# Kernel optimization log

Measured on AMD Instinct MI355X. Metric: run time of the kernel, lower is better.

Reference implementation:

```python
import jax, jax.numpy as jnp
import numpy as np

EPS = 1e-5

def batchnorm2d(x, w, b):
    # training-mode BN: per-channel stats over (B, H, W), biased variance
    mean = jnp.mean(x, axis=(0, 2, 3), keepdims=True)
    var = jnp.var(x, axis=(0, 2, 3), keepdims=True)
    xn = (x - mean) * jax.lax.rsqrt(var + EPS)
    return xn * w[None, :, None, None] + b[None, :, None, None]

def setup_inputs() -> dict:
    key = jax.random.key(0)
    ks = jax.random.split(key, 12)
    B, C, H, W = 4, 64, 64, 64
    Cq = C // 8
    s = 1.0 / np.sqrt(C)
    return {
        "x": jax.random.normal(ks[0], (B, C, H, W), jnp.float32),
        "Wq": jax.random.normal(ks[1], (Cq, C), jnp.float32) * s,
        "bq": jnp.zeros((Cq,), jnp.float32),
        "Wk": jax.random.normal(ks[2], (Cq, C), jnp.float32) * s,
        "bk": jnp.zeros((Cq,), jnp.float32),
        "Wv": jax.random.normal(ks[3], (C, C), jnp.float32) * s,
        "bv": jnp.zeros((C,), jnp.float32),
        "gamma_p": jax.random.normal(ks[4], (), jnp.float32) * 0.1,
        "bnp_w": jnp.ones((C,), jnp.float32),
        "bnp_b": jnp.zeros((C,), jnp.float32),
        "gamma_c": jax.random.normal(ks[5], (), jnp.float32) * 0.1,
        "bnc_w": jnp.ones((C,), jnp.float32),
        "bnc_b": jnp.zeros((C,), jnp.float32),
    }

def reference(x, Wq, bq, Wk, bk, Wv, bv, gamma_p, bnp_w, bnp_b, gamma_c, bnc_w, bnc_b):
    B, C, H, W = x.shape
    N = H * W
    xf = x.reshape(B, C, N)

    # ---- PAM (position attention) ----
    q = jnp.einsum('dc,bcn->bnd', Wq, xf) + bq  # [B, N, Cq]
    k = jnp.einsum('dc,bcn->bdn', Wk, xf) + bk[None, :, None]  # [B, Cq, N]
    v = jnp.einsum('dc,bcn->bdn', Wv, xf) + bv[None, :, None]  # [B, C, N]
    energy = jnp.einsum('bnd,bdm->bnm', q, k)  # [B, N, N]
    attn = jax.nn.softmax(energy, axis=-1)
    # out[b,c,m] = sum_n v[b,c,n] * attn[m,n]  (bmm(v, attn^T))
    out = jnp.einsum('bcn,bmn->bcm', v, attn).reshape(B, C, H, W)
    out = gamma_p * out
    out = batchnorm2d(out, bnp_w, bnp_b)
    y = out + x  # PAM residual

    # ---- CAM (channel attention) ----
    yf = y.reshape(B, C, N)
    energy_c = jnp.einsum('bcn,bdn->bcd', yf, yf)  # [B, C, C]
    energy_new = jnp.max(energy_c, axis=-1, keepdims=True) - energy_c
    attn_c = jax.nn.softmax(energy_new, axis=-1)
    out_c = jnp.einsum('bcd,bdn->bcn', attn_c, yf).reshape(B, C, H, W)
    out_c = gamma_c * out_c
    out_c = batchnorm2d(out_c, bnc_w, bnc_b)
    return out_c + y  # CAM residual
```

## Files before the change

kernel.cpp:

```cpp
#include <hip/hip_runtime.h>

#define NN 4096
#define EPS 1e-5f

typedef unsigned long long u64;
union f2u { float f[2]; u64 u; };
typedef float f32x2 __attribute__((ext_vector_type(2)));
typedef float f32x4v __attribute__((ext_vector_type(4)));

#define PK_LO(acc, a, b) \
  asm("v_pk_fma_f32 %0, %1, %2, %0 op_sel:[0,0,0] op_sel_hi:[1,0,1]" \
      : "+v"(acc) : "v"(a), "v"(b))
#define PK_HI(acc, a, b) \
  asm("v_pk_fma_f32 %0, %1, %2, %0 op_sel:[0,1,0] op_sel_hi:[1,1,1]" \
      : "+v"(acc) : "v"(a), "v"(b))

#define Q_OFF   0u
#define K_OFF   131072u
#define V_OFF   262144u
#define O_OFF   1310720u
#define Y_OFF   2359296u
#define OC_OFF  3407872u
#define AT_OFF  4456448u
#define S2_OFF  4472832u
#define PS_OFF  4472960u
#define CNT_OFF 4473088u
#define OP_OFF  4473344u
#define LP_OFF  8667648u

__global__ __launch_bounds__(256) void proj_kernel(
    const float* __restrict__ x, const float* __restrict__ Wq, const float* __restrict__ bq,
    const float* __restrict__ Wk, const float* __restrict__ bk,
    const float* __restrict__ Wv, const float* __restrict__ bv,
    float* __restrict__ q, float* __restrict__ k, float* __restrict__ v) {
  __shared__ float sWq[8*64], sWk[8*64], sWv[64*64], sbq[8], sbk[8], sbv[64];
  __shared__ float xt[64*68];
  int t = threadIdx.x;
  int b = blockIdx.x >> 6;
  int sp = blockIdx.x & 63;
  int n0 = sp << 6;
  for (int i = t; i < 512; i += 256) { sWq[i] = Wq[i]; sWk[i] = Wk[i]; }
  for (int i = t; i < 4096; i += 256) sWv[i] = Wv[i];
  if (t < 64) sbv[t] = bv[t];
  if (t < 8) { sbq[t] = bq[t]; sbk[t] = bk[t]; }
  for (int i = t; i < 1024; i += 256) {
    int c = i >> 4, nf = (i & 15) << 2;
    *(float4*)&xt[c*68 + nf] =
        *(const float4*)&x[(size_t)(((b<<6)|c)<<12) + n0 + nf];
  }
  __syncthreads();
  int nl = t & 63;
  int n = n0 | nl;
  int cg_ = t >> 6;
  float xv[64];
  #pragma unroll
  for (int c = 0; c < 64; ++c) xv[c] = xt[c*68 + nl];
  for (int c = cg_*16; c < cg_*16+16; ++c) {
    float acc = sbv[c];
    #pragma unroll
    for (int c2 = 0; c2 < 64; ++c2) acc += sWv[c*64 + c2] * xv[c2];
    v[(((b<<6)|c)<<12) | n] = acc;
  }
  if (cg_ == 0) {
    #pragma unroll
    for (int d = 0; d < 8; ++d) {
      float acc = sbq[d];
      #pragma unroll
      for (int c = 0; c < 64; ++c) acc += sWq[d*64+c] * xv[c];
      q[(((b<<12)|n)<<3) | d] = acc;
    }
  } else if (cg_ == 1) {
    #pragma unroll
    for (int d = 0; d < 8; ++d) {
      float acc = sbk[d];
      #pragma unroll
      for (int c = 0; c < 64; ++c) acc += sWk[d*64+c] * xv[c];
      k[(((b<<3)|d)<<12) | n] = acc;
    }
  }
}

__global__ __launch_bounds__(256, 4) void attn_kernel(
    const float* __restrict__ q, const float* __restrict__ k,
    const float* __restrict__ v, float* __restrict__ op,
    float* __restrict__ lp, float* __restrict__ o,
    float* __restrict__ psums, int* __restrict__ cnt) {
  __shared__ float kst[64*12];
  __shared__ float vst[64*68];
  __shared__ float pst[64*68];
  __shared__ int who;

  const int bi   = blockIdx.x;
  const int g    = bi & 3;
  const int rest = bi >> 2;
  const int mt   = rest & 63;
  const int b    = rest >> 6;
  const int m0   = mt << 6;
  const int t    = threadIdx.x;

  const int rq = t & 15;
  const int sg = t >> 4;

  f32x2 qq[2][8];
  {
    f32x4v rowv[4][2];
    #pragma unroll
    for (int r = 0; r < 4; ++r) {
      const f32x4v* qp = (const f32x4v*)&q[(size_t)(((b<<12) | (m0 + (rq<<2) + r)) << 3)];
      rowv[r][0] = qp[0]; rowv[r][1] = qp[1];
    }
    #pragma unroll
    for (int p = 0; p < 2; ++p)
      #pragma unroll
      for (int j = 0; j < 8; ++j) {
        f32x2 w;
        w[0] = rowv[2*p][j>>2][j&3];
        w[1] = rowv[2*p+1][j>>2][j&3];
        qq[p][j] = w;
      }
  }

  float lsum[4] = {0.f, 0.f, 0.f, 0.f};
  f32x2 A2[4][2];
  #pragma unroll
  for (int c = 0; c < 4; ++c) { A2[c][0] = (f32x2){0.f,0.f}; A2[c][1] = (f32x2){0.f,0.f}; }

  const int span = NN >> 2;
  const int nbeg = g * span;

  for (int n0 = nbeg; n0 < nbeg + span; n0 += 64) {
    __syncthreads();
    #pragma unroll
    for (int i = t; i < 512; i += 256) {
      int ni = i & 63, d = i >> 6;
      kst[ni*12 + d] = k[(((b<<3)|d)<<12) + n0 + ni];
    }
    #pragma unroll
    for (int i = t; i < 4096; i += 256) {
      int ni = i & 63, c = i >> 6;
      vst[ni*68 + c] = v[(((b<<6)|c)<<12) + n0 + ni];
    }
    __syncthreads();
    #pragma unroll
    for (int j4 = 0; j4 < 4; ++j4) {
      const int ni = (sg << 2) | j4;
      const f32x4v ka = *(const f32x4v*)&kst[ni*12];
      const f32x4v kb = *(const f32x4v*)&kst[ni*12 + 4];
      const f32x2 k01 = __builtin_shufflevector(ka, ka, 0, 1);
      const f32x2 k23 = __builtin_shufflevector(ka, ka, 2, 3);
      const f32x2 k45 = __builtin_shufflevector(kb, kb, 0, 1);
      const f32x2 k67 = __builtin_shufflevector(kb, kb, 2, 3);
      f32x2 s01 = (f32x2){0.f,0.f}, s23 = (f32x2){0.f,0.f};
      PK_LO(s01, qq[0][0], k01); PK_HI(s01, qq[0][1], k01);
      PK_LO(s01, qq[0][2], k23); PK_HI(s01, qq[0][3], k23);
      PK_LO(s01, qq[0][4], k45); PK_HI(s01, qq[0][5], k45);
      PK_LO(s01, qq[0][6], k67); PK_HI(s01, qq[0][7], k67);
      PK_LO(s23, qq[1][0], k01); PK_HI(s23, qq[1][1], k01);
      PK_LO(s23, qq[1][2], k23); PK_HI(s23, qq[1][3], k23);
      PK_LO(s23, qq[1][4], k45); PK_HI(s23, qq[1][5], k45);
      PK_LO(s23, qq[1][6], k67); PK_HI(s23, qq[1][7], k67);
      const float e0 = __expf(s01[0]), e1 = __expf(s01[1]);
      const float e2 = __expf(s23[0]), e3 = __expf(s23[1]);
      lsum[0] += e0; lsum[1] += e1; lsum[2] += e2; lsum[3] += e3;
      *(float4*)&pst[ni*68 + (rq<<2)] = make_float4(e0, e1, e2, e3);
    }
    __syncthreads();
    #pragma unroll 4
    for (int ni = 0; ni < 64; ++ni) {
      const f32x4v p4 = *(const f32x4v*)&pst[ni*68 + (sg<<2)];
      const f32x4v v4 = *(const f32x4v*)&vst[ni*68 + (rq<<2)];
      const f32x2 pa = __builtin_shufflevector(p4, p4, 0, 1);
      const f32x2 pb = __builtin_shufflevector(p4, p4, 2, 3);
      const f32x2 va = __builtin_shufflevector(v4, v4, 0, 1);
      const f32x2 vb = __builtin_shufflevector(v4, v4, 2, 3);
      PK_LO(A2[0][0], pa, va); PK_LO(A2[0][1], pb, va);
      PK_HI(A2[1][0], pa, va); PK_HI(A2[1][1], pb, va);
      PK_LO(A2[2][0], pa, vb); PK_LO(A2[2][1], pb, vb);
      PK_HI(A2[3][0], pa, vb); PK_HI(A2[3][1], pb, vb);
    }
  }
  __syncthreads();
  *(float4*)&pst[sg*68 + (rq<<2)] = make_float4(lsum[0], lsum[1], lsum[2], lsum[3]);
  __syncthreads();
  if (t < 64) {
    float l = 0.f;
    #pragma unroll
    for (int s = 0; s < 16; ++s) l += pst[s*68 + t];
    __hip_atomic_store(&lp[(((((g<<2)|b)<<6) | mt)<<6) | t], l,
                       __ATOMIC_RELAXED, __HIP_MEMORY_SCOPE_AGENT);
  }
  float* ob = op + ((size_t)((((g<<2)|b)<<6) | mt) << 12);
  #pragma unroll
  for (int r = 0; r < 4; ++r) {
    const int base = (((sg<<2)|r)<<6) | (rq<<2);
    const int h = r >> 1, e = r & 1;
    f2u lo, hi;
    lo.f[0] = A2[0][h][e]; lo.f[1] = A2[1][h][e];
    hi.f[0] = A2[2][h][e]; hi.f[1] = A2[3][h][e];
    __hip_atomic_store((u64*)&ob[base],     lo.u, __ATOMIC_RELAXED, __HIP_MEMORY_SCOPE_AGENT);
    __hip_atomic_store((u64*)&ob[base + 2], hi.u, __ATOMIC_RELAXED, __HIP_MEMORY_SCOPE_AGENT);
  }

  __syncthreads();
  if (t == 0)
    who = __hip_atomic_fetch_add(&cnt[(b<<6) | mt], 1,
                                 __ATOMIC_RELEASE, __HIP_MEMORY_SCOPE_AGENT);
  __syncthreads();
  if (who != 3) return;
  if (t == 0)
    __builtin_amdgcn_fence(__ATOMIC_ACQUIRE, "agent");
  __syncthreads();

  float* sm = vst;
  float* linv = kst;
  if (t < 64) {
    float l = 0.f;
    #pragma unroll
    for (int g2 = 0; g2 < 4; ++g2)
      l += lp[(((((g2<<2)|b)<<6) | mt)<<6) | t];
    linv[t] = 1.f / l;
  }
  __syncthreads();
  for (int i = 0; i < 16; ++i) {
    int idx = (i<<8) + t;
    float s = 0.f;
    #pragma unroll
    for (int g2 = 0; g2 < 4; ++g2)
      s += op[((size_t)((((g2<<2)|b)<<6) | mt) << 12) + idx];
    int m = idx >> 6, c = idx & 63;
    sm[c*65 + m] = s * linv[m];
  }
  __syncthreads();
  for (int i = 0; i < 16; ++i) {
    int idx = (i<<8) + t;
    int m = idx & 63, c = idx >> 6;
    float ov = sm[c*65 + m];
    o[(((b<<6)|c)<<12) | (mt<<6) | m] = ov;
    float s1 = ov, s2 = ov*ov;
    #pragma unroll
    for (int off2 = 32; off2; off2 >>= 1) {
      s1 += __shfl_xor(s1, off2, 64);
      s2 += __shfl_xor(s2, off2, 64);
    }
    if ((t & 63) == 0) { atomicAdd(&psums[c], s1); atomicAdd(&psums[64+c], s2); }
  }
}

__global__ __launch_bounds__(256) void yg_kernel(
    const float* __restrict__ o, const float* __restrict__ x,
    const float* __restrict__ psums,
    const float* __restrict__ gp, const float* __restrict__ w1, const float* __restrict__ bb1,
    float* __restrict__ y, float* __restrict__ gpart) {
  __shared__ float yt[64*36];
  __shared__ float cf[128];
  const int bi = blockIdx.x;
  const int b = bi >> 7, sp = bi & 127;
  const int t = threadIdx.x;
  const int n0 = sp << 5;
  if (t < 64) {
    float m1 = psums[t] * (1.f/16384.f), m2 = psums[64+t] * (1.f/16384.f);
    float var = m2 - m1*m1;
    float gg = *gp;
    float r = rsqrtf(gg*gg*var + EPS);
    float a = gg * r * w1[t];
    cf[t] = a; cf[64+t] = bb1[t] - m1*a;
  }
  __syncthreads();
  #pragma unroll
  for (int i = 0; i < 8; ++i) {
    int idx = (i<<8) + t;
    int c = idx >> 5, m = idx & 31;
    size_t gi = ((size_t)(((b<<6)|c)<<12)) + n0 + m;
    float yv = o[gi]*cf[c] + cf[64+c] + x[gi];
    yt[c*36 + m] = yv;
    y[gi] = yv;
  }
  __syncthreads();
  {
    int tc = t >> 4, td = t & 15;
    float acc[4][4] = {{0.f}};
    #pragma unroll
    for (int mj = 0; mj < 8; ++mj) {
      float4 ya[4], yb[4];
      #pragma unroll
      for (int r = 0; r < 4; ++r)  ya[r] = *(const float4*)&yt[((tc<<2)+r)*36 + (mj<<2)];
      #pragma unroll
      for (int ss = 0; ss < 4; ++ss) yb[ss] = *(const float4*)&yt[((td<<2)+ss)*36 + (mj<<2)];
      #pragma unroll
      for (int r = 0; r < 4; ++r)
        #pragma unroll
        for (int ss = 0; ss < 4; ++ss)
          acc[r][ss] += ya[r].x*yb[ss].x + ya[r].y*yb[ss].y + ya[r].z*yb[ss].z + ya[r].w*yb[ss].w;
    }
    float* gb = gpart + ((size_t)bi << 12);
    #pragma unroll
    for (int r = 0; r < 4; ++r)
      *(float4*)&gb[(((tc<<2)+r)<<6) | (td<<2)] =
          make_float4(acc[r][0], acc[r][1], acc[r][2], acc[r][3]);
  }
}

__global__ __launch_bounds__(256) void csm_kernel(
    const float* __restrict__ gpart, float* __restrict__ attnc) {
  __shared__ float red[256];
  const int bi = blockIdx.x;
  const int b = bi >> 6, row = bi & 63;
  const int t = threadIdx.x;
  const int d = t & 63, spg = t >> 6;
  float e = 0.f;
  #pragma unroll
  for (int jj = 0; jj < 32; ++jj) {
    int ch = (spg<<5) + jj;
    e += gpart[((size_t)((b<<7)|ch) << 12) + (row<<6) + d];
  }
  red[t] = e;
  __syncthreads();
  if (t < 64) {
    float ee = red[t]+red[64+t]+red[128+t]+red[192+t];
    float mn = ee;
    #pragma unroll
    for (int off = 32; off; off >>= 1) mn = fminf(mn, __shfl_xor(mn, off, 64));
    float p = __expf(mn - ee);
    float s = p;
    #pragma unroll
    for (int off = 32; off; off >>= 1) s += __shfl_xor(s, off, 64);
    attnc[(((b<<6)|row)<<6) | t] = p / s;
  }
}

__global__ __launch_bounds__(256) void cam_apply_kernel(
    const float* __restrict__ attn, const float* __restrict__ y,
    float* __restrict__ oc, float* __restrict__ sums) {
  __shared__ float satt[64*68];
  const int bi = blockIdx.x;
  const int b = bi >> 7, sp = bi & 127;
  const int n0 = sp << 5;
  const int t = threadIdx.x;
  const int nl = t & 31, cg_ = t >> 5;
  for (int i = t; i < 4096; i += 256)
    satt[(i>>6)*68 + (i&63)] = attn[(b<<12) | i];
  __syncthreads();
  float yv[64];
  #pragma unroll
  for (int d = 0; d < 64; ++d)
    yv[d] = y[((size_t)(((b<<6)|d)<<12)) + n0 + nl];
  #pragma unroll
  for (int j = 0; j < 8; ++j) {
    int c = (cg_<<3) + j;
    float acc = 0.f;
    #pragma unroll
    for (int d4 = 0; d4 < 16; ++d4) {
      float4 avv = *(const float4*)&satt[c*68 + (d4<<2)];
      acc += avv.x*yv[d4*4] + avv.y*yv[d4*4+1] + avv.z*yv[d4*4+2] + avv.w*yv[d4*4+3];
    }
    oc[((size_t)(((b<<6)|c)<<12)) + n0 + nl] = acc;
    float s1 = acc, s2 = acc*acc;
    #pragma unroll
    for (int off = 16; off; off >>= 1) {
      s1 += __shfl_xor(s1, off, 64);
      s2 += __shfl_xor(s2, off, 64);
    }
    if ((t & 31) == 0) { atomicAdd(&sums[c], s1); atomicAdd(&sums[64+c], s2); }
  }
}

__global__ __launch_bounds__(256) void fin_kernel(
    const float* __restrict__ oc, const float* __restrict__ y,
    const float* __restrict__ s2b,
    const float* __restrict__ gc, const float* __restrict__ w2, const float* __restrict__ bb2,
    float* __restrict__ out) {
  __shared__ float cf[128];
  const int t = threadIdx.x;
  if (t < 64) {
    float m1 = s2b[t] * (1.f/16384.f), m2 = s2b[64+t] * (1.f/16384.f);
    float var = m2 - m1*m1;
    float gg = *gc;
    float r = rsqrtf(gg*gg*var + EPS);
    float a = gg * r * w2[t];
    cf[t] = a; cf[64+t] = bb2[t] - m1*a;
  }
  __syncthreads();
  const int off = (blockIdx.x*256 + t) << 2;
  const int c = (off >> 12) & 63;
  const float a = cf[c], bb = cf[64+c];
  const float4 o4 = *(const float4*)&oc[off];
  const float4 y4 = *(const float4*)&y[off];
  float4 r4;
  r4.x = o4.x*a + bb + y4.x;
  r4.y = o4.y*a + bb + y4.y;
  r4.z = o4.z*a + bb + y4.z;
  r4.w = o4.w*a + bb + y4.w;
  *(float4*)&out[off] = r4;
}

extern "C" void kernel_launch(void* const* d_in, const int* in_sizes, int n_in,
                              void* d_out, int out_size, void* d_ws, size_t ws_size,
                              hipStream_t stream) {
  (void)in_sizes; (void)n_in; (void)out_size; (void)ws_size;
  const float* x      = (const float*)d_in[0];
  const float* Wq     = (const float*)d_in[1];
  const float* bq     = (const float*)d_in[2];
  const float* Wk     = (const float*)d_in[3];
  const float* bk     = (const float*)d_in[4];
  const float* Wv     = (const float*)d_in[5];
  const float* bv     = (const float*)d_in[6];
  const float* gp     = (const float*)d_in[7];
  const float* bnp_w  = (const float*)d_in[8];
  const float* bnp_b  = (const float*)d_in[9];
  const float* gc     = (const float*)d_in[10];
  const float* bnc_w  = (const float*)d_in[11];
  const float* bnc_b  = (const float*)d_in[12];

  float* ws = (float*)d_ws;
  float* q     = ws + Q_OFF;
  float* k     = ws + K_OFF;
  float* v     = ws + V_OFF;
  float* o     = ws + O_OFF;
  float* y     = ws + Y_OFF;
  float* oc    = ws + OC_OFF;
  float* atc   = ws + AT_OFF;
  float* s2b   = ws + S2_OFF;
  float* ps    = ws + PS_OFF;
  int*   cnt   = (int*)(ws + CNT_OFF);
  float* op    = ws + OP_OFF;
  float* lpart = ws + LP_OFF;
  float* gpart = op;

  hipMemsetAsync(s2b, 0, 512u * sizeof(float), stream);

  proj_kernel<<<256, 256, 0, stream>>>(x, Wq, bq, Wk, bk, Wv, bv, q, k, v);
  attn_kernel<<<1024, 256, 0, stream>>>(q, k, v, op, lpart, o, ps, cnt);
  yg_kernel<<<512, 256, 0, stream>>>(o, x, ps, gp, bnp_w, bnp_b, y, gpart);
  csm_kernel<<<256, 256, 0, stream>>>(gpart, atc);
  cam_apply_kernel<<<512, 256, 0, stream>>>(atc, y, oc, s2b);
  fin_kernel<<<1024, 256, 0, stream>>>(oc, y, s2b, gc, bnc_w, bnc_b, (float*)d_out);
}
```

Baseline: 459.3 us.

## Split PV accumulation over waves with larger 8x8 register tiles and LDS reduction

Each wave now handles a quarter of the 64-key chunk and each thread accumulates an 8x8 (m x c) tile instead of 4x4, which doubles FMAs per LDS load. The four per-wave partial tiles are then summed through LDS in a two-step tree reduction, and the result is staged in LDS before the global store. This trades higher register pressure (64 accumulator floats) and extra barriers and reduction traffic for less LDS read bandwidth in the inner loop.

New measurement: 659.2 us. 43.5% more time.

```diff
diff --git a/kernel.cpp b/kernel.cpp
--- a/kernel.cpp
+++ b/kernel.cpp
@@ -100,6 +100,10 @@
 
   const int rq = t & 15;
   const int sg = t >> 4;
+  const int wv = t >> 6;
+  const int li = t & 63;
+  const int mg = li & 7;
+  const int cgp = li >> 3;
 
   f32x2 qq[2][8];
   {
@@ -121,9 +125,11 @@
   }
 
   float lsum[4] = {0.f, 0.f, 0.f, 0.f};
-  f32x2 A2[4][2];
-  #pragma unroll
-  for (int c = 0; c < 4; ++c) { A2[c][0] = (f32x2){0.f,0.f}; A2[c][1] = (f32x2){0.f,0.f}; }
+  f32x2 A2[8][4];
+  #pragma unroll
+  for (int c = 0; c < 8; ++c)
+    #pragma unroll
+    for (int mp = 0; mp < 4; ++mp) A2[c][mp] = (f32x2){0.f, 0.f};
 
   const int span = NN >> 2;
   const int nbeg = g * span;
@@ -166,21 +172,87 @@
     }
     __syncthreads();
     #pragma unroll 4
-    for (int ni = 0; ni < 64; ++ni) {
-      const f32x4v p4 = *(const f32x4v*)&pst[ni*68 + (sg<<2)];
-      const f32x4v v4 = *(const f32x4v*)&vst[ni*68 + (rq<<2)];
-      const f32x2 pa = __builtin_shufflevector(p4, p4, 0, 1);
-      const f32x2 pb = __builtin_shufflevector(p4, p4, 2, 3);
-      const f32x2 va = __builtin_shufflevector(v4, v4, 0, 1);
-      const f32x2 vb = __builtin_shufflevector(v4, v4, 2, 3);
-      PK_LO(A2[0][0], pa, va); PK_LO(A2[0][1], pb, va);
-      PK_HI(A2[1][0], pa, va); PK_HI(A2[1][1], pb, va);
-      PK_LO(A2[2][0], pa, vb); PK_LO(A2[2][1], pb, vb);
-      PK_HI(A2[3][0], pa, vb); PK_HI(A2[3][1], pb, vb);
-    }
-  }
-  __syncthreads();
+    for (int i = 0; i < 16; ++i) {
+      const int ni = (wv << 4) + i;
+      const f32x4v pa = *(const f32x4v*)&pst[ni*68 + (mg<<3)];
+      const f32x4v pb = *(const f32x4v*)&pst[ni*68 + (mg<<3) + 4];
+      const f32x4v va = *(const f32x4v*)&vst[ni*68 + (cgp<<3)];
+      const f32x4v vb = *(const f32x4v*)&vst[ni*68 + (cgp<<3) + 4];
+      const f32x2 p01 = __builtin_shufflevector(pa, pa, 0, 1);
+      const f32x2 p23 = __builtin_shufflevector(pa, pa, 2, 3);
+      const f32x2 p45 = __builtin_shufflevector(pb, pb, 0, 1);
+      const f32x2 p67 = __builtin_shufflevector(pb, pb, 2, 3);
+      const f32x2 v01 = __builtin_shufflevector(va, va, 0, 1);
+      const f32x2 v23 = __builtin_shufflevector(va, va, 2, 3);
+      const f32x2 v45 = __builtin_shufflevector(vb, vb, 0, 1);
+      const f32x2 v67 = __builtin_shufflevector(vb, vb, 2, 3);
+      PK_LO(A2[0][0], p01, v01); PK_LO(A2[0][1], p23, v01);
+      PK_LO(A2[0][2], p45, v01); PK_LO(A2[0][3], p67, v01);
+      PK_HI(A2[1][0], p01, v01); PK_HI(A2[1][1], p23, v01);
+      PK_HI(A2[1][2], p45, v01); PK_HI(A2[1][3], p67, v01);
+      PK_LO(A2[2][0], p01, v23); PK_LO(A2[2][1], p23, v23);
+      PK_LO(A2[2][2], p45, v23); PK_LO(A2[2][3], p67, v23);
+      PK_HI(A2[3][0], p01, v23); PK_HI(A2[3][1], p23, v23);
+      PK_HI(A2[3][2], p45, v23); PK_HI(A2[3][3], p67, v23);
+      PK_LO(A2[4][0], p01, v45); PK_LO(A2[4][1], p23, v45);
+      PK_LO(A2[4][2], p45, v45); PK_LO(A2[4][3], p67, v45);
+      PK_HI(A2[5][0], p01, v45); PK_HI(A2[5][1], p23, v45);
+      PK_HI(A2[5][2], p45, v45); PK_HI(A2[5][3], p67, v45);
+      PK_LO(A2[6][0], p01, v67); PK_LO(A2[6][1], p23, v67);
+      PK_LO(A2[6][2], p45, v67); PK_LO(A2[6][3], p67, v67);
+      PK_HI(A2[7][0], p01, v67); PK_HI(A2[7][1], p23, v67);
+      PK_HI(A2[7][2], p45, v67); PK_HI(A2[7][3], p67, v67);
+    }
+  }
+  __syncthreads();
+  {
+    #define PUBLISH(buf)                                                        \
+      { _Pragma("unroll")                                                       \
+        for (int c = 0; c < 8; ++c) {                                           \
+          f32x4v lo = __builtin_shufflevector(A2[c][0], A2[c][1], 0,1,2,3);     \
+          f32x4v hi = __builtin_shufflevector(A2[c][2], A2[c][3], 0,1,2,3);     \
+          *(f32x4v*)&(buf)[li*68 + (c<<3)]     = lo;                            \
+          *(f32x4v*)&(buf)[li*68 + (c<<3) + 4] = hi;                            \
+        } }
+    #define ACCUM(buf)                                                          \
+      { _Pragma("unroll")                                                       \
+        for (int c = 0; c < 8; ++c) {                                           \
+          f32x4v lo = *(const f32x4v*)&(buf)[li*68 + (c<<3)];                   \
+          f32x4v hi = *(const f32x4v*)&(buf)[li*68 + (c<<3) + 4];               \
+          A2[c][0][0] += lo[0]; A2[c][0][1] += lo[1];                           \
+          A2[c][1][0] += lo[2]; A2[c][1][1] += lo[3];                           \
+          A2[c][2][0] += hi[0]; A2[c][2][1] += hi[1];                           \
+          A2[c][3][0] += hi[2]; A2[c][3][1] += hi[3];                           \
+        } }
+    if (wv == 2) PUBLISH(pst);
+    if (wv == 3) PUBLISH(vst);
+    __syncthreads();
+    if (wv == 0) ACCUM(pst);
+    if (wv == 1) ACCUM(vst);
+    __syncthreads();
+    if (wv == 1) PUBLISH(pst);
+    __syncthreads();
+    if (wv == 0) ACCUM(pst);
+    __syncthreads();
+    #undef PUBLISH
+    #undef ACCUM
+  }
   *(float4*)&pst[sg*68 + (rq<<2)] = make_float4(lsum[0], lsum[1], lsum[2], lsum[3]);
+  if (wv == 0) {
+    #pragma unroll
+    for (int mp = 0; mp < 4; ++mp)
+      #pragma unroll
+      for (int e = 0; e < 2; ++e) {
+        const int row = (mg<<3) + (mp<<1) + e;
+        f32x4v w0, w1;
+        w0[0] = A2[0][mp][e]; w0[1] = A2[1][mp][e];
+        w0[2] = A2[2][mp][e]; w0[3] = A2[3][mp][e];
+        w1[0] = A2[4][mp][e]; w1[1] = A2[5][mp][e];
+        w1[2] = A2[6][mp][e]; w1[3] = A2[7][mp][e];
+        *(f32x4v*)&vst[row*68 + (cgp<<3)]     = w0;
+        *(f32x4v*)&vst[row*68 + (cgp<<3) + 4] = w1;
+      }
+  }
   __syncthreads();
   if (t < 64) {
     float l = 0.f;
@@ -192,11 +264,12 @@
   float* ob = op + ((size_t)((((g<<2)|b)<<6) | mt) << 12);
   #pragma unroll
   for (int r = 0; r < 4; ++r) {
-    const int base = (((sg<<2)|r)<<6) | (rq<<2);
-    const int h = r >> 1, e = r & 1;
+    const int m = (sg<<2) | r;
+    const float4 vv = *(const float4*)&vst[m*68 + (rq<<2)];
+    const int base = (m<<6) | (rq<<2);
     f2u lo, hi;
-    lo.f[0] = A2[0][h][e]; lo.f[1] = A2[1][h][e];
-    hi.f[0] = A2[2][h][e]; hi.f[1] = A2[3][h][e];
+    lo.f[0] = vv.x; lo.f[1] = vv.y;
+    hi.f[0] = vv.z; hi.f[1] = vv.w;
     __hip_atomic_store((u64*)&ob[base],     lo.u, __ATOMIC_RELAXED, __HIP_MEMORY_SCOPE_AGENT);
     __hip_atomic_store((u64*)&ob[base + 2], hi.u, __ATOMIC_RELAXED, __HIP_MEMORY_SCOPE_AGENT);
   }
```

## Split PV accumulation across n halves with larger 8x4 per-thread tiles and LDS reduction

Applied to the files above, without the earlier changes.

The P·V inner loop now gives each thread an 8-row by 4-channel output tile instead of 4x4. The two halves of the block each handle half of the 64 n-values per tile. This raises FMA-per-LDS-load reuse. The partial accumulators are then reduced through shared memory before only half the threads write the output. The change adds registers (16 packed accumulators), an extra LDS round trip with two barriers, and idle threads during the store phase.

Result: slower. 469.1 us (+2.2%).

```diff
diff --git a/kernel.cpp b/kernel.cpp
--- a/kernel.cpp
+++ b/kernel.cpp
@@ -100,6 +100,12 @@
 
   const int rq = t & 15;
   const int sg = t >> 4;
+  const int wv = t >> 6;
+  const int li = t & 63;
+  const int h   = wv >> 1;
+  const int li2 = ((wv & 1) << 6) | li;
+  const int mg = li2 >> 4;
+  const int cq = li2 & 15;
 
   f32x2 qq[2][8];
   {
@@ -121,9 +127,11 @@
   }
 
   float lsum[4] = {0.f, 0.f, 0.f, 0.f};
-  f32x2 A2[4][2];
-  #pragma unroll
-  for (int c = 0; c < 4; ++c) { A2[c][0] = (f32x2){0.f,0.f}; A2[c][1] = (f32x2){0.f,0.f}; }
+  f32x2 A2[4][4];
+  #pragma unroll
+  for (int c = 0; c < 4; ++c)
+    #pragma unroll
+    for (int mp = 0; mp < 4; ++mp) A2[c][mp] = (f32x2){0.f, 0.f};
 
   const int span = NN >> 2;
   const int nbeg = g * span;
@@ -166,17 +174,49 @@
     }
     __syncthreads();
     #pragma unroll 4
-    for (int ni = 0; ni < 64; ++ni) {
-      const f32x4v p4 = *(const f32x4v*)&pst[ni*68 + (sg<<2)];
-      const f32x4v v4 = *(const f32x4v*)&vst[ni*68 + (rq<<2)];
-      const f32x2 pa = __builtin_shufflevector(p4, p4, 0, 1);
-      const f32x2 pb = __builtin_shufflevector(p4, p4, 2, 3);
-      const f32x2 va = __builtin_shufflevector(v4, v4, 0, 1);
-      const f32x2 vb = __builtin_shufflevector(v4, v4, 2, 3);
-      PK_LO(A2[0][0], pa, va); PK_LO(A2[0][1], pb, va);
-      PK_HI(A2[1][0], pa, va); PK_HI(A2[1][1], pb, va);
-      PK_LO(A2[2][0], pa, vb); PK_LO(A2[2][1], pb, vb);
-      PK_HI(A2[3][0], pa, vb); PK_HI(A2[3][1], pb, vb);
+    for (int i = 0; i < 32; ++i) {
+      const int ni = (h << 5) + i;
+      const f32x4v pa = *(const f32x4v*)&pst[ni*68 + (mg<<3)];
+      const f32x4v pb = *(const f32x4v*)&pst[ni*68 + (mg<<3) + 4];
+      const f32x4v va = *(const f32x4v*)&vst[ni*68 + (cq<<2)];
+      const f32x2 p01 = __builtin_shufflevector(pa, pa, 0, 1);
+      const f32x2 p23 = __builtin_shufflevector(pa, pa, 2, 3);
+      const f32x2 p45 = __builtin_shufflevector(pb, pb, 0, 1);
+      const f32x2 p67 = __builtin_shufflevector(pb, pb, 2, 3);
+      const f32x2 v01 = __builtin_shufflevector(va, va, 0, 1);
+      const f32x2 v23 = __builtin_shufflevector(va, va, 2, 3);
+      PK_LO(A2[0][0], p01, v01); PK_LO(A2[0][1], p23, v01);
+      PK_LO(A2[0][2], p45, v01); PK_LO(A2[0][3], p67, v01);
+      PK_HI(A2[1][0], p01, v01); PK_HI(A2[1][1], p23, v01);
+      PK_HI(A2[1][2], p45, v01); PK_HI(A2[1][3], p67, v01);
+      PK_LO(A2[2][0], p01, v23); PK_LO(A2[2][1], p23, v23);
+      PK_LO(A2[2][2], p45, v23); PK_LO(A2[2][3], p67, v23);
+      PK_HI(A2[3][0], p01, v23); PK_HI(A2[3][1], p23, v23);
+      PK_HI(A2[3][2], p45, v23); PK_HI(A2[3][3], p67, v23);
+    }
+  }
+  __syncthreads();
+  if (h == 1) {
+    float* buf = (wv == 2) ? pst : vst;
+    #pragma unroll
+    for (int c = 0; c < 4; ++c) {
+      f32x4v lo = __builtin_shufflevector(A2[c][0], A2[c][1], 0,1,2,3);
+      f32x4v hi = __builtin_shufflevector(A2[c][2], A2[c][3], 0,1,2,3);
+      *(f32x4v*)&buf[li*34 + (c<<3)]     = lo;
+      *(f32x4v*)&buf[li*34 + (c<<3) + 4] = hi;
+    }
+  }
+  __syncthreads();
+  if (h == 0) {
+    const float* buf = (wv == 0) ? pst : vst;
+    #pragma unroll
+    for (int c = 0; c < 4; ++c) {
+      f32x4v lo = *(const f32x4v*)&buf[li*34 + (c<<3)];
+      f32x4v hi = *(const f32x4v*)&buf[li*34 + (c<<3) + 4];
+      A2[c][0][0] += lo[0]; A2[c][0][1] += lo[1];
+      A2[c][1][0] += lo[2]; A2[c][1][1] += lo[3];
+      A2[c][2][0] += hi[0]; A2[c][2][1] += hi[1];
+      A2[c][3][0] += hi[2]; A2[c][3][1] += hi[3];
     }
   }
   __syncthreads();
@@ -189,16 +229,20 @@
     __hip_atomic_store(&lp[(((((g<<2)|b)<<6) | mt)<<6) | t], l,
                        __ATOMIC_RELAXED, __HIP_MEMORY_SCOPE_AGENT);
   }
-  float* ob = op + ((size_t)((((g<<2)|b)<<6) | mt) << 12);
-  #pragma unroll
-  for (int r = 0; r < 4; ++r) {
-    const int base = (((sg<<2)|r)<<6) | (rq<<2);
-    const int h = r >> 1, e = r & 1;
-    f2u lo, hi;
-    lo.f[0] = A2[0][h][e]; lo.f[1] = A2[1][h][e];
-    hi.f[0] = A2[2][h][e]; hi.f[1] = A2[3][h][e];
-    __hip_atomic_store((u64*)&ob[base],     lo.u, __ATOMIC_RELAXED, __HIP_MEMORY_SCOPE_AGENT);
-    __hip_atomic_store((u64*)&ob[base + 2], hi.u, __ATOMIC_RELAXED, __HIP_MEMORY_SCOPE_AGENT);
+  if (h == 0) {
+    float* ob = op + ((size_t)((((g<<2)|b)<<6) | mt) << 12);
+    #pragma unroll
+    for (int mp = 0; mp < 4; ++mp)
+      #pragma unroll
+      for (int e = 0; e < 2; ++e) {
+        const int row = (mg<<3) + (mp<<1) + e;
+        const int base = (row<<6) | (cq<<2);
+        f2u lo, hi;
+        lo.f[0] = A2[0][mp][e]; lo.f[1] = A2[1][mp][e];
+        hi.f[0] = A2[2][mp][e]; hi.f[1] = A2[3][mp][e];
+        __hip_atomic_store((u64*)&ob[base],     lo.u, __ATOMIC_RELAXED, __HIP_MEMORY_SCOPE_AGENT);
+        __hip_atomic_store((u64*)&ob[base + 2], hi.u, __ATOMIC_RELAXED, __HIP_MEMORY_SCOPE_AGENT);
+      }
   }
 
   __syncthreads();
```
